# Kernel optimization log

Hardware: AMD Instinct MI355X
Metric: run time of the kernel (lower is better)

Reference implementation:

```python
import jax, jax.numpy as jnp
import numpy as np

B, N, DIM = 4, 1024, 768
H, GP = 12, 64
HD = DIM // H
SCALE = HD ** -0.5


def setup_inputs() -> dict:
    key = jax.random.key(0)
    ks = jax.random.split(key, 7)
    s = DIM ** -0.5
    return {
        "x": jax.random.normal(ks[0], (B, N, DIM), dtype=jnp.float32),
        "W_qkv": jax.random.normal(ks[1], (3 * DIM, DIM), dtype=jnp.float32) * s,
        "b_qkv": jnp.zeros((3 * DIM,), dtype=jnp.float32),
        "W_gp": jax.random.normal(ks[2], (GP, DIM), dtype=jnp.float32) * s,
        "alpha": jax.random.normal(ks[3], (1, H, 1, 1), dtype=jnp.float32),
        "W_proj": jax.random.normal(ks[4], (DIM, DIM), dtype=jnp.float32) * s,
        "b_proj": jnp.zeros((DIM,), dtype=jnp.float32),
    }


def reference(x, W_qkv, b_qkv, W_gp, alpha, W_proj, b_proj):
    b, n, c = x.shape
    # qkv projection, split into heads: [b, h, n, hd]
    qkv = x @ W_qkv.T + b_qkv
    q, k, v = jnp.split(qkv, 3, axis=-1)
    def to_heads(t):
        return t.reshape(b, n, H, HD).transpose(0, 2, 1, 3)
    q, k, v = to_heads(q), to_heads(k), to_heads(v)

    # raw attention scores [b, h, n, n]
    attn = jnp.einsum('bhnd,bhmd->bhnm', q, k) * SCALE

    # group similarity: gp weight viewed as [h, gp, hd]
    gp = W_gp.reshape(H, GP, HD)
    gw = jnp.einsum('bhnd,hmd->bhnm', v, gp)          # [b, h, n, gp]
    gw = jax.nn.gelu(gw, approximate=False)           # exact GELU (torch default)
    gw = jax.nn.softmax(gw, axis=-1)
    G = jnp.einsum('bhnm,bhkm->bhnk', gw, gw)         # [b, h, n, n]

    # gated combination
    attn = jax.nn.softmax(attn * G, axis=-1)
    a = jax.nn.sigmoid(alpha)                          # [1, h, 1, 1]
    A = (1.0 - a) * attn + a * G
    # column-sum renormalization (sum over query dim 2)
    A = A / (A.sum(axis=2, keepdims=True) + 1e-8)

    out = jnp.einsum('bhnm,bhmd->bhnd', A, v)
    out = out.transpose(0, 2, 1, 3).reshape(b, n, c)
    return out @ W_proj.T + b_proj
```

## Files before the change

### kernel.cpp

```cpp
#include <hip/hip_runtime.h>
#include <math.h>

namespace {

constexpr int kN   = 1024;
constexpr int kDim = 768;
constexpr int kH   = 12;
constexpr int kBH  = 48;
constexpr float kScale = 0.125f;

typedef __attribute__((ext_vector_type(8))) short short8;
typedef __attribute__((ext_vector_type(4))) short short4v;
typedef __attribute__((ext_vector_type(4))) float f32x4;
typedef __attribute__((ext_vector_type(16))) float f32x16;
typedef __attribute__((ext_vector_type(4))) uint uint4v;
typedef _Float16 f16x8 __attribute__((ext_vector_type(8)));

#define MFMA(a, b, c)      __builtin_amdgcn_mfma_f32_16x16x32_bf16(a, b, c, 0, 0, 0)
#define MFMA32(a, b, c)    __builtin_amdgcn_mfma_f32_32x32x16_bf16(a, b, c, 0, 0, 0)
#define MFMA32F16(a, b, c) __builtin_amdgcn_mfma_f32_32x32x16_f16(a, b, c, 0, 0, 0)

__device__ __forceinline__ ushort f2bf(float f) {
  uint u = __builtin_bit_cast(uint, f);
  u += 0x7fffu + ((u >> 16) & 1u);
  return (ushort)(u >> 16);
}
__device__ __forceinline__ float bf2f(ushort h) {
  uint u = ((uint)h) << 16;
  return __builtin_bit_cast(float, u);
}
__device__ __forceinline__ void split8(const float* f, short8& hi, short8& lo) {
  #pragma unroll
  for (int i = 0; i < 8; i++) {
    const ushort h = f2bf(f[i]);
    hi[i] = (short)h;
    lo[i] = (short)f2bf(f[i] - bf2f(h));
  }
}
__device__ __forceinline__ uint packbf(float a, float b) {
  return (uint)f2bf(a) | ((uint)f2bf(b) << 16);
}
__device__ __forceinline__ ushort f2h(float f) {
  return __builtin_bit_cast(ushort, (_Float16)f);
}

__device__ __forceinline__ void gl16(const void* g, void* l) {
  __builtin_amdgcn_global_load_lds(
      (const __attribute__((address_space(1))) void*)g,
      (__attribute__((address_space(3))) void*)l, 16, 0, 0);
}

__device__ __forceinline__ short8 frag(const short* t, int row, int chunk) {
  return *(const short8*)(t + row * 64 + ((chunk ^ (row & 7)) << 3));
}

template<int ROWS, int W>
__device__ __forceinline__ void stage_tile(short* dst, const short* src,
                                           int stride, int w, int l) {
  #pragma unroll
  for (int c = 0; c < ROWS / 8; c += W) {
    const int cc = c + w;
    const int row0 = cc << 3;
    const int row = row0 + (l >> 3);
    const int ch = (l & 7) ^ (row & 7);
    gl16(src + (size_t)row * stride + (ch << 3), dst + row0 * 64);
  }
}

__global__ __launch_bounds__(256) void k_split(const float* __restrict__ src,
                                               short* __restrict__ h,
                                               short* __restrict__ l) {
  const size_t i = ((size_t)blockIdx.x * 256 + threadIdx.x) * 4;
  const float4 f = *(const float4*)(src + i);
  const float ff[4] = {f.x, f.y, f.z, f.w};
  short4v hv, lv;
  #pragma unroll
  for (int j = 0; j < 4; j++) {
    const ushort u = f2bf(ff[j]);
    hv[j] = (short)u;
    lv[j] = (short)f2bf(ff[j] - bf2f(u));
  }
  *(short4v*)(h + i) = hv;
  *(short4v*)(l + i) = lv;
}

__global__ __launch_bounds__(512) void k_qkv(const short* __restrict__ xh,
                                             const short* __restrict__ xl,
                                             const short* __restrict__ wh,
                                             const short* __restrict__ wl,
                                             const float* __restrict__ bias,
                                             short* __restrict__ qh, short* __restrict__ ql,
                                             short* __restrict__ kh, short* __restrict__ kl,
                                             short* __restrict__ vh, short* __restrict__ vl) {
  __shared__ __align__(16) short sb[32768];
  const int bx = blockIdx.x, by = blockIdx.y;
  const int tid = threadIdx.x, w = tid >> 6, lane = tid & 63;
  const int wr = w >> 2, wc = w & 3;
  const short* Asrc_h = xh + (size_t)(by * 128) * kDim;
  const short* Asrc_l = xl + (size_t)(by * 128) * kDim;
  const short* Bsrc_h = wh + (size_t)(bx * 128) * kDim;
  const short* Bsrc_l = wl + (size_t)(bx * 128) * kDim;

  f32x4 acc[4][2] = {};
  #pragma unroll 1
  for (int t = 0; t < 12; ++t) {
    const int k0 = t * 64;
    __syncthreads();
    stage_tile<128, 8>(sb,         Asrc_h + k0, kDim, w, lane);
    stage_tile<128, 8>(sb + 8192,  Asrc_l + k0, kDim, w, lane);
    stage_tile<128, 8>(sb + 16384, Bsrc_h + k0, kDim, w, lane);
    stage_tile<128, 8>(sb + 24576, Bsrc_l + k0, kDim, w, lane);
    __syncthreads();
    #pragma unroll
    for (int s = 0; s < 2; ++s) {
      const int ch = (s << 2) + (lane >> 4);
      short8 af[4], alf[4], bf_[2], blf[2];
      #pragma unroll
      for (int i = 0; i < 4; i++) {
        const int ar = wr * 64 + i * 16 + (lane & 15);
        af[i]  = frag(sb, ar, ch);
        alf[i] = frag(sb + 8192, ar, ch);
      }
      #pragma unroll
      for (int j = 0; j < 2; j++) {
        const int br = wc * 32 + j * 16 + (lane & 15);
        bf_[j] = frag(sb + 16384, br, ch);
        blf[j] = frag(sb + 24576, br, ch);
      }
      #pragma unroll
      for (int i = 0; i < 4; i++)
        #pragma unroll
        for (int j = 0; j < 2; j++) {
          acc[i][j] = MFMA(af[i], bf_[j], acc[i][j]);
          acc[i][j] = MFMA(af[i], blf[j], acc[i][j]);
          acc[i][j] = MFMA(alf[i], bf_[j], acc[i][j]);
        }
    }
  }
  #pragma unroll
  for (int j = 0; j < 2; j++) {
    const int col = bx * 128 + wc * 32 + j * 16 + (lane & 15);
    const int part = col / 768;
    const int rem = col - part * 768;
    const int hh = rem >> 6, d = rem & 63;
    short* dh = (part == 0) ? qh : ((part == 1) ? kh : vh);
    short* dl = (part == 0) ? ql : ((part == 1) ? kl : vl);
    const float bv = bias[col];
    const float scl = (part == 0) ? kScale : 1.0f;
    #pragma unroll
    for (int i = 0; i < 4; i++) {
      #pragma unroll
      for (int r = 0; r < 4; r++) {
        const int gr = by * 128 + wr * 64 + i * 16 + ((lane >> 4) << 2) + r;
        const int b = gr >> 10, n = gr & 1023;
        const float val = (acc[i][j][r] + bv) * scl;
        const ushort hu = f2bf(val);
        const size_t idx = (size_t)((b * kH + hh) * kN + n) * 64 + d;
        dh[idx] = (short)hu;
        dl[idx] = (short)f2bf(val - bf2f(hu));
      }
    }
  }
}

__global__ __launch_bounds__(512) void k_gw(const short* __restrict__ vh,
                                            const short* __restrict__ vl,
                                            const float* __restrict__ Wgp,
                                            short* __restrict__ gwh,
                                            short* __restrict__ gwl) {
  const int bh = blockIdx.x;
  const int h = bh % kH;
  const int n0 = blockIdx.y << 7;
  const int tid = threadIdx.x, w = tid >> 6, lane = tid & 63;
  __shared__ __align__(16) short gph[4096], gpl[4096];
  {
    const int r = tid >> 3, c = tid & 7;
    float f[8] __attribute__((aligned(16)));
    *(float4*)(f + 0) = *(const float4*)(Wgp + h * 4096 + r * 64 + c * 8);
    *(float4*)(f + 4) = *(const float4*)(Wgp + h * 4096 + r * 64 + c * 8 + 4);
    short8 hh, ll;
    split8(f, hh, ll);
    const int slot = c ^ (r & 7);
    *(short8*)(gph + r * 64 + slot * 8) = hh;
    *(short8*)(gpl + r * 64 + slot * 8) = ll;
  }
  short8 vhf[2], vlf[2];
  const size_t arow = (size_t)(bh * kN + n0 + w * 16 + (lane & 15)) * 64 + ((lane >> 4) << 3);
  vhf[0] = *(const short8*)(vh + arow); vhf[1] = *(const short8*)(vh + arow + 32);
  vlf[0] = *(const short8*)(vl + arow); vlf[1] = *(const short8*)(vl + arow + 32);
  __syncthreads();

  f32x4 aU[4] = {};
  #pragma unroll
  for (int msub = 0; msub < 4; msub++) {
    #pragma unroll
    for (int s = 0; s < 2; s++) {
      const int row = (msub << 4) + (lane & 15);
      const int ch = (s << 2) + (lane >> 4);
      const short8 bh_ = frag(gph, row, ch);
      const short8 bl_ = frag(gpl, row, ch);
      aU[msub] = MFMA(vhf[s], bh_, aU[msub]);
      aU[msub] = MFMA(vhf[s], bl_, aU[msub]);
      aU[msub] = MFMA(vlf[s], bh_, aU[msub]);
    }
  }
  #pragma unroll
  for (int r = 0; r < 4; r++) {
    float u[4];
    #pragma unroll
    for (int m = 0; m < 4; m++) {
      const float a = aU[m][r];
      u[m] = 0.5f * a * (1.0f + erff(a * 0.70710678118654752f));
    }
    float mx = fmaxf(fmaxf(u[0], u[1]), fmaxf(u[2], u[3]));
    #pragma unroll
    for (int msk = 1; msk < 16; msk <<= 1) mx = fmaxf(mx, __shfl_xor(mx, msk));
    float e[4], ssum = 0.f;
    #pragma unroll
    for (int m = 0; m < 4; m++) { e[m] = __expf(u[m] - mx); ssum += e[m]; }
    #pragma unroll
    for (int msk = 1; msk < 16; msk <<= 1) ssum += __shfl_xor(ssum, msk);
    const float inv = 1.0f / ssum;
    const int n = n0 + w * 16 + ((lane >> 4) << 2) + r;
    #pragma unroll
    for (int m = 0; m < 4; m++) {
      const float g = e[m] * inv;
      const ushort hu = f2bf(g);
      const size_t idx = (size_t)(bh * kN + n) * 64 + (m << 4) + (lane & 15);
      gwh[idx] = (short)hu;
      gwl[idx] = (short)f2bf(g - bf2f(hu));
    }
  }
}

template<int F16>
__global__ __launch_bounds__(256) void k_vt(const short* __restrict__ vh,
                                            const float* __restrict__ rcolv,
                                            short* __restrict__ vtg) {
  const int bh = blockIdx.x;
  const int n0 = blockIdx.y << 6;
  __shared__ short t[64][80];
  const int tid = threadIdx.x;
  {
    const int n = tid >> 2, d0 = (tid & 3) << 4;
    const float rc = rcolv[bh * kN + n0 + n];
    const short8 a = *(const short8*)(vh + (size_t)(bh * kN + n0 + n) * 64 + d0);
    const short8 b = *(const short8*)(vh + (size_t)(bh * kN + n0 + n) * 64 + d0 + 8);
    #pragma unroll
    for (int i = 0; i < 8; ++i) {
      const float v0 = bf2f((ushort)a[i]) * rc;
      const float v1 = bf2f((ushort)b[i]) * rc;
      t[d0 + i][n]     = F16 ? (short)f2h(v0) : (short)f2bf(v0);
      t[d0 + 8 + i][n] = F16 ? (short)f2h(v1) : (short)f2bf(v1);
    }
  }
  __syncthreads();
  const int d = tid >> 2, j0 = (tid & 3) << 4;
  short* dst = vtg + (size_t)bh * 65536 + (size_t)d * 1024 + n0 + j0;
  *(short8*)(dst)     = *(const short8*)(&t[d][j0]);
  *(short8*)(dst + 8) = *(const short8*)(&t[d][j0 + 8]);
}

__global__ __launch_bounds__(256, 3) void k_denom(const short* __restrict__ qh,
                                                  const short* __restrict__ ql,
                                                  const short* __restrict__ kh,
                                                  const short* __restrict__ kl,
                                                  const short* __restrict__ gwh,
                                                  const short* __restrict__ gwl,
                                                  float* __restrict__ rdenom) {
  const int bh = blockIdx.x;
  const int n0 = blockIdx.y << 6;
  const int tid = threadIdx.x, w = tid >> 6, lane = tid & 63;
  const int lc = lane & 31, hl = lane >> 5;
  const int nw = w & 1, mh = w >> 1;
  __shared__ __align__(16) short sb[16384];
  __shared__ float part[4][32];

  short8 qB[4], qlB[4], gB[4], glB[4];
  {
    const size_t nrow = (size_t)(bh * kN + n0 + nw * 32 + lc) * 64;
    #pragma unroll
    for (int ks = 0; ks < 4; ks++) {
      const int off = ks * 16 + (hl << 3);
      qB[ks]  = *(const short8*)(qh  + nrow + off);
      qlB[ks] = *(const short8*)(ql  + nrow + off);
      gB[ks]  = *(const short8*)(gwh + nrow + off);
      glB[ks] = *(const short8*)(gwl + nrow + off);
    }
  }
  float dsum = 0.f;
  #pragma unroll 1
  for (int t = 0; t < 16; ++t) {
    __syncthreads();
    const size_t mo0 = (size_t)(bh * kN + t * 32) * 64;
    const size_t mo1 = (size_t)(bh * kN + 512 + t * 32) * 64;
    stage_tile<32, 4>(sb,                kh  + mo0, 64, w, lane);
    stage_tile<32, 4>(sb + 2048,         kh  + mo1, 64, w, lane);
    stage_tile<32, 4>(sb + 4096,         kl  + mo0, 64, w, lane);
    stage_tile<32, 4>(sb + 4096 + 2048,  kl  + mo1, 64, w, lane);
    stage_tile<32, 4>(sb + 8192,         gwh + mo0, 64, w, lane);
    stage_tile<32, 4>(sb + 8192 + 2048,  gwh + mo1, 64, w, lane);
    stage_tile<32, 4>(sb + 12288,        gwl + mo0, 64, w, lane);
    stage_tile<32, 4>(sb + 12288 + 2048, gwl + mo1, 64, w, lane);
    __syncthreads();
    f32x16 aS = {}, aG = {};
    #pragma unroll
    for (int ks = 0; ks < 4; ++ks) {
      const int row = mh * 32 + lc;
      const int ck = ks * 2 + hl;
      const short8 Ah_ = frag(sb, row, ck);
      const short8 Al_ = frag(sb + 4096, row, ck);
      const short8 Eh_ = frag(sb + 8192, row, ck);
      const short8 El_ = frag(sb + 12288, row, ck);
      aS = MFMA32(Ah_, qB[ks], aS);
      aS = MFMA32(Al_, qB[ks], aS);
      aS = MFMA32(Ah_, qlB[ks], aS);
      aG = MFMA32(Eh_, gB[ks], aG);
      aG = MFMA32(El_, gB[ks], aG);
      aG = MFMA32(Eh_, glB[ks], aG);
    }
    #pragma unroll
    for (int r = 0; r < 16; ++r)
      dsum += __expf(aS[r] * aG[r]);
  }
  dsum += __shfl_xor(dsum, 32);
  if (hl == 0) part[w][lc] = dsum;
  __syncthreads();
  if (tid < 64)
    rdenom[bh * kN + n0 + tid] =
        1.0f / (part[tid >> 5][tid & 31] + part[2 + (tid >> 5)][tid & 31]);
}

template<int WA>
__global__ __launch_bounds__(256, 3) void k_colsum(const short* __restrict__ qh,
                                                   const short* __restrict__ ql,
                                                   const short* __restrict__ kh,
                                                   const short* __restrict__ kl,
                                                   const short* __restrict__ gwh,
                                                   const short* __restrict__ gwl,
                                                   const float* __restrict__ rdenom,
                                                   const float* __restrict__ alpha,
                                                   float* __restrict__ rcolv,
                                                   ushort* __restrict__ Ab) {
  const int bh = blockIdx.x;
  const int m0 = blockIdx.y << 6;
  const int tid = threadIdx.x, w = tid >> 6, lane = tid & 63;
  const int lc = lane & 31, hl = lane >> 5;
  const int mw = w & 1, nh = w >> 1;
  __shared__ __align__(16) short sb[16384];
  __shared__ float part[4][32];
  __shared__ float rdl[2][32];
  const float ah_ = 1.0f / (1.0f + __expf(-alpha[bh % kH]));
  const float om = 1.0f - ah_;
  const int m_g = m0 + mw * 32 + lc;
  ushort* Arow = WA ? (Ab + ((size_t)bh << 20) + m_g) : nullptr;

  short8 kB[4], klB[4], gB[4], glB[4];
  {
    const size_t mrow = (size_t)(bh * kN + m_g) * 64;
    #pragma unroll
    for (int ks = 0; ks < 4; ks++) {
      const int off = ks * 16 + (hl << 3);
      kB[ks]  = *(const short8*)(kh  + mrow + off);
      klB[ks] = *(const short8*)(kl  + mrow + off);
      gB[ks]  = *(const short8*)(gwh + mrow + off);
      glB[ks] = *(const short8*)(gwl + mrow + off);
    }
  }
  float csum = 0.f;
  #pragma unroll 1
  for (int t = 0; t < 16; ++t) {
    __syncthreads();
    const size_t no0 = (size_t)(bh * kN + t * 32) * 64;
    const size_t no1 = (size_t)(bh * kN + 512 + t * 32) * 64;
    stage_tile<32, 4>(sb,                qh  + no0, 64, w, lane);
    stage_tile<32, 4>(sb + 2048,         qh  + no1, 64, w, lane);
    stage_tile<32, 4>(sb + 4096,         ql  + no0, 64, w, lane);
    stage_tile<32, 4>(sb + 4096 + 2048,  ql  + no1, 64, w, lane);
    stage_tile<32, 4>(sb + 8192,         gwh + no0, 64, w, lane);
    stage_tile<32, 4>(sb + 8192 + 2048,  gwh + no1, 64, w, lane);
    stage_tile<32, 4>(sb + 12288,        gwl + no0, 64, w, lane);
    stage_tile<32, 4>(sb + 12288 + 2048, gwl + no1, 64, w, lane);
    if (tid < 64)
      rdl[tid >> 5][tid & 31] =
          rdenom[bh * kN + (tid >> 5) * 512 + t * 32 + (tid & 31)];
    __syncthreads();
    f32x16 aS = {}, aG = {};
    #pragma unroll
    for (int ks = 0; ks < 4; ++ks) {
      const int row = nh * 32 + lc;
      const int ck = ks * 2 + hl;
      const short8 Ah_ = frag(sb, row, ck);
      const short8 Al_ = frag(sb + 4096, row, ck);
      const short8 Eh_ = frag(sb + 8192, row, ck);
      const short8 El_ = frag(sb + 12288, row, ck);
      aS = MFMA32(Ah_, kB[ks], aS);
      aS = MFMA32(Al_, kB[ks], aS);
      aS = MFMA32(Ah_, klB[ks], aS);
      aG = MFMA32(Eh_, gB[ks], aG);
      aG = MFMA32(El_, gB[ks], aG);
      aG = MFMA32(Eh_, glB[ks], aG);
    }
    #pragma unroll
    for (int r = 0; r < 16; ++r) {
      const int nr = (r & 3) + ((r >> 2) << 3) + (hl << 2);
      const float g = aG[r];
      const float a = om * (__expf(aS[r] * g) * rdl[nh][nr]) + ah_ * g;
      csum += a;
      if (WA) {
        const int n_g = nh * 512 + t * 32 + nr;
        Arow[(size_t)n_g << 10] = f2h(a);
      }
    }
  }
  csum += __shfl_xor(csum, 32);
  if (hl == 0) part[w][lc] = csum;
  __syncthreads();
  if (tid < 64)
    rcolv[bh * kN + m0 + tid] =
        1.0f / (part[tid >> 5][tid & 31] + part[2 + (tid >> 5)][tid & 31] + 1e-8f);
}

__global__ __launch_bounds__(256) void k_outA(const ushort* __restrict__ Ab,
                                              const short* __restrict__ vtf,
                                              short* __restrict__ ctxh,
                                              short* __restrict__ ctxl) {
  const int bh = blockIdx.x;
  const int h = bh % kH;
  const int b = bh / kH;
  const int n0 = blockIdx.y << 6;
  const int tid = threadIdx.x, w = tid >> 6, lane = tid & 63;
  const int lc = lane & 31, hl = lane >> 5;
  const int nw = w & 1, mh = w >> 1;
  __shared__ __align__(16) short sbm[10240];
  short* At = sbm;
  short* Vt = sbm + 4096;
  const ushort* Abh = Ab + ((size_t)bh << 20);
  const short* Vbh = vtf + ((size_t)bh << 16);
  f32x16 oac[2] = {};

  #pragma unroll 1
  for (int t = 0; t < 16; ++t) {
    __syncthreads();
    #pragma unroll
    for (int c = 0; c < 8; c += 4) {
      const int cc = c + w;
      const int row0 = cc << 3;
      const int row = row0 + (lane >> 3);
      const int ce = (lane & 7) ^ (row & 7);
      const int mg = ((ce >> 2) ? 512 : 0) + t * 32 + ((ce & 3) << 3);
      gl16(Abh + ((size_t)(n0 + row) << 10) + mg, At + row0 * 64);
      gl16(Vbh + ((size_t)row << 10) + mg, Vt + row0 * 64);
    }
    __syncthreads();
    #pragma unroll
    for (int dt = 0; dt < 2; ++dt)
      #pragma unroll
      for (int ks = 0; ks < 2; ++ks) {
        const int ck = mh * 4 + ks * 2 + hl;
        const f16x8 va = __builtin_bit_cast(f16x8, frag(Vt, dt * 32 + lc, ck));
        const f16x8 pe = __builtin_bit_cast(f16x8, frag(At, nw * 32 + lc, ck));
        oac[dt] = MFMA32F16(va, pe, oac[dt]);
      }
  }
  __syncthreads();
  float* buf = (float*)sbm;
  if (mh == 1) {
    #pragma unroll
    for (int dt = 0; dt < 2; ++dt)
      #pragma unroll
      for (int r = 0; r < 16; ++r) {
        const int d = dt * 32 + (r & 3) + ((r >> 2) << 3) + (hl << 2);
        buf[(nw * 32 + lc) * 68 + d] = oac[dt][r];
      }
  }
  __syncthreads();
  if (mh == 0) {
    #pragma unroll
    for (int dt = 0; dt < 2; ++dt)
      #pragma unroll
      for (int r = 0; r < 16; ++r) {
        const int d = dt * 32 + (r & 3) + ((r >> 2) << 3) + (hl << 2);
        const int idx = (nw * 32 + lc) * 68 + d;
        buf[idx] = oac[dt][r] + buf[idx];
      }
  }
  __syncthreads();
  {
    const int rowi = tid >> 2;
    const int d0 = (tid & 3) << 4;
    float f[16] __attribute__((aligned(16)));
    #pragma unroll
    for (int j = 0; j < 4; ++j)
      *(float4*)(f + 4 * j) = *(const float4*)(&buf[rowi * 68 + d0 + 4 * j]);
    const int n = n0 + rowi;
    short* dsth = ctxh + (size_t)(b * kN + n) * kDim + h * 64 + d0;
    short* dstl = ctxl + (size_t)(b * kN + n) * kDim + h * 64 + d0;
    #pragma unroll
    for (int g8 = 0; g8 < 2; ++g8) {
      short8 hi, lo;
      split8(f + 8 * g8, hi, lo);
      *(short8*)(dsth + 8 * g8) = hi;
      *(short8*)(dstl + 8 * g8) = lo;
    }
  }
}

__global__ __launch_bounds__(256, 3) void k_out9(const short* __restrict__ qh,
                                                 const short* __restrict__ ql,
                                                 const short* __restrict__ kh,
                                                 const short* __restrict__ kl,
                                                 const short* __restrict__ vtg,
                                                 const short* __restrict__ gwh,
                                                 const short* __restrict__ gwl,
                                                 const float* __restrict__ rdenom,
                                                 const float* __restrict__ alpha,
                                                 short* __restrict__ ctxh,
                                                 short* __restrict__ ctxl) {
  const int bh = blockIdx.x;
  const int h = bh % kH;
  const int b = bh / kH;
  const int n0 = blockIdx.y << 6;
  const int tid = threadIdx.x, w = tid >> 6, lane = tid & 63;
  const int lc = lane & 31, hl = lane >> 5;
  const int nw = w & 1, mh = w >> 1;
  __shared__ __align__(16) short sb[20480];
  const float ah_ = 1.0f / (1.0f + __expf(-alpha[h]));
  const float om = 1.0f - ah_;

  short8 qB[4], qlB[4], gB[4], glB[4];
  {
    const size_t nrow = (size_t)(bh * kN + n0 + nw * 32 + lc) * 64;
    #pragma unroll
    for (int ks = 0; ks < 4; ks++) {
      const int off = ks * 16 + (hl << 3);
      qB[ks]  = *(const short8*)(qh  + nrow + off);
      qlB[ks] = *(const short8*)(ql  + nrow + off);
      gB[ks]  = *(const short8*)(gwh + nrow + off);
      glB[ks] = *(const short8*)(gwl + nrow + off);
    }
  }
  const float rdn = rdenom[bh * kN + n0 + nw * 32 + lc];
  const short* vbh = vtg + (size_t)bh * 65536;
  f32x16 oac[2] = {};

  #pragma unroll 1
  for (int t = 0; t < 16; ++t) {
    __syncthreads();
    const size_t mo0 = (size_t)(bh * kN + t * 32) * 64;
    const size_t mo1 = (size_t)(bh * kN + 512 + t * 32) * 64;
    stage_tile<32, 4>(sb,                kh  + mo0, 64, w, lane);
    stage_tile<32, 4>(sb + 2048,         kh  + mo1, 64, w, lane);
    stage_tile<32, 4>(sb + 4096,         kl  + mo0, 64, w, lane);
    stage_tile<32, 4>(sb + 4096 + 2048,  kl  + mo1, 64, w, lane);
    stage_tile<32, 4>(sb + 8192,         gwh + mo0, 64, w, lane);
    stage_tile<32, 4>(sb + 8192 + 2048,  gwh + mo1, 64, w, lane);
    stage_tile<32, 4>(sb + 12288,        gwl + mo0, 64, w, lane);
    stage_tile<32, 4>(sb + 12288 + 2048, gwl + mo1, 64, w, lane);
    #pragma unroll
    for (int c = 0; c < 8; c += 4) {
      const int cc = c + w;
      const int row0 = cc << 3;
      const int row = row0 + (lane >> 3);
      const int ch = (lane & 7) ^ (row & 7);
      const int mg = ((ch >> 2) ? 512 : 0) + t * 32 + ((ch & 3) << 3);
      gl16(vbh + (size_t)row * 1024 + mg, sb + 16384 + row0 * 64);
    }
    __syncthreads();
    f32x16 aS = {}, aG = {};
    #pragma unroll
    for (int ks = 0; ks < 4; ++ks) {
      const int row = mh * 32 + lc;
      const int ck = ks * 2 + hl;
      const short8 Ah_ = frag(sb, row, ck);
      const short8 Al_ = frag(sb + 4096, row, ck);
      const short8 Eh_ = frag(sb + 8192, row, ck);
      const short8 El_ = frag(sb + 12288, row, ck);
      aS = MFMA32(Ah_, qB[ks], aS);
      aS = MFMA32(Al_, qB[ks], aS);
      aS = MFMA32(Ah_, qlB[ks], aS);
      aG = MFMA32(Eh_, gB[ks], aG);
      aG = MFMA32(El_, gB[ks], aG);
      aG = MFMA32(Eh_, glB[ks], aG);
    }
    float a[16];
    #pragma unroll
    for (int r = 0; r < 16; ++r) {
      const float g = aG[r];
      const float p = __expf(aS[r] * g) * rdn;
      a[r] = om * p + ah_ * g;
    }
    short8 pf[2];
    {
      uint W[8], Ws[8];
      #pragma unroll
      for (int j = 0; j < 8; ++j) W[j] = packbf(a[2 * j], a[2 * j + 1]);
      #pragma unroll
      for (int j = 0; j < 8; ++j) Ws[j] = __shfl_xor(W[j], 32);
      uint4v b0, b1;
      b0[0] = hl ? Ws[2] : W[0];  b0[1] = hl ? Ws[3] : W[1];
      b0[2] = hl ? W[2]  : Ws[0]; b0[3] = hl ? W[3]  : Ws[1];
      b1[0] = hl ? Ws[6] : W[4];  b1[1] = hl ? Ws[7] : W[5];
      b1[2] = hl ? W[6]  : Ws[4]; b1[3] = hl ? W[7]  : Ws[5];
      pf[0] = __builtin_bit_cast(short8, b0);
      pf[1] = __builtin_bit_cast(short8, b1);
    }
    #pragma unroll
    for (int dt = 0; dt < 2; ++dt)
      #pragma unroll
      for (int ks = 0; ks < 2; ++ks) {
        const short8 va = frag(sb + 16384, dt * 32 + lc, mh * 4 + ks * 2 + hl);
        oac[dt] = MFMA32(va, pf[ks], oac[dt]);
      }
  }
  __syncthreads();
  float* buf = (float*)sb;
  if (mh == 1) {
    #pragma unroll
    for (int dt = 0; dt < 2; ++dt)
      #pragma unroll
      for (int r = 0; r < 16; ++r) {
        const int d = dt * 32 + (r & 3) + ((r >> 2) << 3) + (hl << 2);
        buf[(nw * 32 + lc) * 68 + d] = oac[dt][r];
      }
  }
  __syncthreads();
  if (mh == 0) {
    #pragma unroll
    for (int dt = 0; dt < 2; ++dt)
      #pragma unroll
      for (int r = 0; r < 16; ++r) {
        const int d = dt * 32 + (r & 3) + ((r >> 2) << 3) + (hl << 2);
        const int idx = (nw * 32 + lc) * 68 + d;
        buf[idx] = oac[dt][r] + buf[idx];
      }
  }
  __syncthreads();
  {
    const int rowi = tid >> 2;
    const int d0 = (tid & 3) << 4;
    float f[16] __attribute__((aligned(16)));
    #pragma unroll
    for (int j = 0; j < 4; ++j)
      *(float4*)(f + 4 * j) = *(const float4*)(&buf[rowi * 68 + d0 + 4 * j]);
    const int n = n0 + rowi;
    short* dsth = ctxh + (size_t)(b * kN + n) * kDim + h * 64 + d0;
    short* dstl = ctxl + (size_t)(b * kN + n) * kDim + h * 64 + d0;
    #pragma unroll
    for (int g8 = 0; g8 < 2; ++g8) {
      short8 hi, lo;
      split8(f + 8 * g8, hi, lo);
      *(short8*)(dsth + 8 * g8) = hi;
      *(short8*)(dstl + 8 * g8) = lo;
    }
  }
}

__global__ __launch_bounds__(512) void k_proj(const short* __restrict__ ch_,
                                              const short* __restrict__ cl_,
                                              const short* __restrict__ wh,
                                              const short* __restrict__ wl,
                                              const float* __restrict__ bias,
                                              float* __restrict__ out) {
  __shared__ __align__(16) short sb[2][32768];
  const int bx = blockIdx.x, by = blockIdx.y;
  const int tid = threadIdx.x, w = tid >> 6, lane = tid & 63;
  const int wr = w >> 2, wc = w & 3;
  const short* Asrc_h = ch_ + (size_t)(by * 128) * kDim;
  const short* Asrc_l = cl_ + (size_t)(by * 128) * kDim;
  const short* Bsrc_h = wh + (size_t)(bx * 128) * kDim;
  const short* Bsrc_l = wl + (size_t)(bx * 128) * kDim;

  f32x4 acc[4][2] = {};
  {
    short* nb = sb[0];
    stage_tile<128, 8>(nb,         Asrc_h, kDim, w, lane);
    stage_tile<128, 8>(nb + 8192,  Asrc_l, kDim, w, lane);
    stage_tile<128, 8>(nb + 16384, Bsrc_h, kDim, w, lane);
    stage_tile<128, 8>(nb + 24576, Bsrc_l, kDim, w, lane);
  }
  int p = 0;
  #pragma unroll 1
  for (int t = 0; t < 12; ++t) {
    __syncthreads();
    if (t < 11) {
      const int k0 = (t + 1) * 64;
      short* nb = sb[p ^ 1];
      stage_tile<128, 8>(nb,         Asrc_h + k0, kDim, w, lane);
      stage_tile<128, 8>(nb + 8192,  Asrc_l + k0, kDim, w, lane);
      stage_tile<128, 8>(nb + 16384, Bsrc_h + k0, kDim, w, lane);
      stage_tile<128, 8>(nb + 24576, Bsrc_l + k0, kDim, w, lane);
    }
    const short* cb = sb[p];
    #pragma unroll
    for (int s = 0; s < 2; ++s) {
      const int ch = (s << 2) + (lane >> 4);
      short8 af[4], alf[4], bf_[2], blf[2];
      #pragma unroll
      for (int i = 0; i < 4; i++) {
        const int ar = wr * 64 + i * 16 + (lane & 15);
        af[i]  = frag(cb, ar, ch);
        alf[i] = frag(cb + 8192, ar, ch);
      }
      #pragma unroll
      for (int j = 0; j < 2; j++) {
        const int br = wc * 32 + j * 16 + (lane & 15);
        bf_[j] = frag(cb + 16384, br, ch);
        blf[j] = frag(cb + 24576, br, ch);
      }
      #pragma unroll
      for (int i = 0; i < 4; i++)
        #pragma unroll
        for (int j = 0; j < 2; j++) {
          acc[i][j] = MFMA(af[i], bf_[j], acc[i][j]);
          acc[i][j] = MFMA(af[i], blf[j], acc[i][j]);
          acc[i][j] = MFMA(alf[i], bf_[j], acc[i][j]);
          acc[i][j] = MFMA(alf[i], blf[j], acc[i][j]);
        }
    }
    p ^= 1;
  }
  #pragma unroll
  for (int j = 0; j < 2; j++) {
    const int col = bx * 128 + wc * 32 + j * 16 + (lane & 15);
    const float bv = bias[col];
    #pragma unroll
    for (int i = 0; i < 4; i++) {
      #pragma unroll
      for (int r = 0; r < 4; r++) {
        const int row = by * 128 + wr * 64 + i * 16 + ((lane >> 4) << 2) + r;
        out[(size_t)row * kDim + col] = acc[i][j][r] + bv;
      }
    }
  }
}

}

extern "C" void kernel_launch(void* const* d_in, const int* in_sizes, int n_in,
                              void* d_out, int out_size, void* d_ws, size_t ws_size,
                              hipStream_t stream) {
  const float* x     = (const float*)d_in[0];
  const float* Wqkv  = (const float*)d_in[1];
  const float* bqkv  = (const float*)d_in[2];
  const float* Wgp   = (const float*)d_in[3];
  const float* alpha = (const float*)d_in[4];
  const float* Wproj = (const float*)d_in[5];
  const float* bproj = (const float*)d_in[6];
  float* out = (float*)d_out;

  const size_t he = 3145728;
  short* qh  = (short*)d_ws;
  short* ql  = qh + he;
  short* kh  = ql + he;
  short* kl  = kh + he;
  short* vh  = kl + he;
  short* vl  = vh + he;
  short* gwh = vl + he;
  short* gwl = gwh + he;
  short* xh  = gwl + he;
  short* xl  = xh + he;
  float* rdenom = (float*)(xl + he);
  float* rcolv  = rdenom + (size_t)kBH * kN;
  ushort* Ab    = (ushort*)(rcolv + (size_t)kBH * kN);
  const size_t need_mat = (size_t)(rcolv + (size_t)kBH * kN - (float*)d_ws) * 4
                        + (size_t)kBH * kN * kN * 2;
  const bool mat = ws_size >= need_mat;

  short* Wqh = gwh;  short* Wql = gwl;
  short* vt  = vl;
  short* ctxh = xh;  short* ctxl = xl;
  short* Wph = qh;   short* Wpl = ql;

  k_split<<<3072, 256, 0, stream>>>(x, xh, xl);
  k_split<<<1728, 256, 0, stream>>>(Wqkv, Wqh, Wql);
  k_qkv  <<<dim3(18, 32), 512, 0, stream>>>(xh, xl, Wqh, Wql, bqkv,
                                            qh, ql, kh, kl, vh, vl);
  k_gw   <<<dim3(kBH, 8), 512, 0, stream>>>(vh, vl, Wgp, gwh, gwl);
  k_denom<<<dim3(kBH, 16), 256, 0, stream>>>(qh, ql, kh, kl, gwh, gwl, rdenom);
  if (mat) {
    k_colsum<1><<<dim3(kBH, 16), 256, 0, stream>>>(qh, ql, kh, kl, gwh, gwl,
                                                   rdenom, alpha, rcolv, Ab);
    k_vt<1> <<<dim3(kBH, 16), 256, 0, stream>>>(vh, rcolv, vt);
    k_outA  <<<dim3(kBH, 16), 256, 0, stream>>>(Ab, vt, ctxh, ctxl);
  } else {
    k_colsum<0><<<dim3(kBH, 16), 256, 0, stream>>>(qh, ql, kh, kl, gwh, gwl,
                                                   rdenom, alpha, rcolv, nullptr);
    k_vt<0> <<<dim3(kBH, 16), 256, 0, stream>>>(vh, rcolv, vt);
    k_out9  <<<dim3(kBH, 16), 256, 0, stream>>>(qh, ql, kh, kl, vt, gwh, gwl,
                                                rdenom, alpha, ctxh, ctxl);
  }
  k_split<<<576, 256, 0, stream>>>(Wproj, Wph, Wpl);
  k_proj <<<dim3(6, 32), 512, 0, stream>>>(ctxh, ctxl, Wph, Wpl, bproj, out);
}
```

Baseline: 228.9 us.

## Store exp scores once and factor the G term through a low-rank product

The materialized path now has the denominator pass write unnormalized exp(S*G) scores in fp16 and per-block column partials. This replaces the second full QK/G recomputation that the column-sum kernel used to do. The column normalizer is built from those partials plus a closed-form sum over G using the gw column sums. In the output, the alpha*G*V term is factored as gw·(gw^T·V') via a small per-head 64x64 matrix M, so it no longer goes through the n×n matrix. The cost is extra kernels (transpose, rcol, M), an fp16 exp matrix that uses a fixed -4 shift and could overflow or underflow, and a re-read of E for the column partials.

```diff
diff --git a/kernel.cpp b/kernel.cpp
--- a/kernel.cpp
+++ b/kernel.cpp
@@ -42,6 +42,9 @@
 }
 __device__ __forceinline__ ushort f2h(float f) {
   return __builtin_bit_cast(ushort, (_Float16)f);
+}
+__device__ __forceinline__ float h2f(ushort u) {
+  return (float)__builtin_bit_cast(_Float16, u);
 }
 
 __device__ __forceinline__ void gl16(const void* g, void* l) {
@@ -167,7 +170,8 @@
                                             const short* __restrict__ vl,
                                             const float* __restrict__ Wgp,
                                             short* __restrict__ gwh,
-                                            short* __restrict__ gwl) {
+                                            short* __restrict__ gwl,
+                                            short* __restrict__ gwf) {
   const int bh = blockIdx.x;
   const int h = bh % kH;
   const int n0 = blockIdx.y << 7;
@@ -229,8 +233,36 @@
       const size_t idx = (size_t)(bh * kN + n) * 64 + (m << 4) + (lane & 15);
       gwh[idx] = (short)hu;
       gwl[idx] = (short)f2bf(g - bf2f(hu));
-    }
-  }
+      if (gwf) gwf[idx] = (short)f2h(g);
+    }
+  }
+}
+
+__global__ __launch_bounds__(256) void k_gwt(const short* __restrict__ gwh,
+                                             const short* __restrict__ gwl,
+                                             short* __restrict__ gwt) {
+  const int bh = blockIdx.x;
+  const int n0 = blockIdx.y << 6;
+  __shared__ short t[64][80];
+  const int tid = threadIdx.x;
+  {
+    const int n = tid >> 2, k0 = (tid & 3) << 4;
+    const size_t row = (size_t)(bh * kN + n0 + n) * 64 + k0;
+    const short8 h0 = *(const short8*)(gwh + row);
+    const short8 h1 = *(const short8*)(gwh + row + 8);
+    const short8 l0 = *(const short8*)(gwl + row);
+    const short8 l1 = *(const short8*)(gwl + row + 8);
+    #pragma unroll
+    for (int i = 0; i < 8; ++i) {
+      t[k0 + i][n]     = (short)f2h(bf2f((ushort)h0[i]) + bf2f((ushort)l0[i]));
+      t[k0 + 8 + i][n] = (short)f2h(bf2f((ushort)h1[i]) + bf2f((ushort)l1[i]));
+    }
+  }
+  __syncthreads();
+  const int k = tid >> 2, j0 = (tid & 3) << 4;
+  short* dst = gwt + ((size_t)bh << 16) + (size_t)k * 1024 + n0 + j0;
+  *(short8*)(dst)     = *(const short8*)(&t[k][j0]);
+  *(short8*)(dst + 8) = *(const short8*)(&t[k][j0 + 8]);
 }
 
 template<int F16>
@@ -259,6 +291,312 @@
   short* dst = vtg + (size_t)bh * 65536 + (size_t)d * 1024 + n0 + j0;
   *(short8*)(dst)     = *(const short8*)(&t[d][j0]);
   *(short8*)(dst + 8) = *(const short8*)(&t[d][j0 + 8]);
+}
+
+__global__ __launch_bounds__(256, 3) void k_denomE(const short* __restrict__ qh,
+                                                   const short* __restrict__ ql,
+                                                   const short* __restrict__ kh,
+                                                   const short* __restrict__ kl,
+                                                   const short* __restrict__ gwh,
+                                                   const short* __restrict__ gwl,
+                                                   float* __restrict__ rdenom,
+                                                   ushort* __restrict__ Eb,
+                                                   float* __restrict__ partials) {
+  const int bh = blockIdx.x;
+  const int blk = blockIdx.y;
+  const int n0 = blk << 6;
+  const int tid = threadIdx.x, w = tid >> 6, lane = tid & 63;
+  const int lc = lane & 31, hl = lane >> 5;
+  const int nw = w & 1, mh = w >> 1;
+  __shared__ __align__(16) short sb[16384];
+  __shared__ float part[4][32];
+  __shared__ float rdl[64];
+
+  short8 qB[4], qlB[4], gB[4], glB[4];
+  {
+    const size_t nrow = (size_t)(bh * kN + n0 + nw * 32 + lc) * 64;
+    #pragma unroll
+    for (int ks = 0; ks < 4; ks++) {
+      const int off = ks * 16 + (hl << 3);
+      qB[ks]  = *(const short8*)(qh  + nrow + off);
+      qlB[ks] = *(const short8*)(ql  + nrow + off);
+      gB[ks]  = *(const short8*)(gwh + nrow + off);
+      glB[ks] = *(const short8*)(gwl + nrow + off);
+    }
+  }
+  ushort* Ebh = Eb + ((size_t)bh << 20);
+  float dsum[16] = {};
+  #pragma unroll 1
+  for (int t = 0; t < 16; ++t) {
+    __syncthreads();
+    const size_t mo0 = (size_t)(bh * kN + t * 32) * 64;
+    const size_t mo1 = (size_t)(bh * kN + 512 + t * 32) * 64;
+    stage_tile<32, 4>(sb,                kh  + mo0, 64, w, lane);
+    stage_tile<32, 4>(sb + 2048,         kh  + mo1, 64, w, lane);
+    stage_tile<32, 4>(sb + 4096,         kl  + mo0, 64, w, lane);
+    stage_tile<32, 4>(sb + 4096 + 2048,  kl  + mo1, 64, w, lane);
+    stage_tile<32, 4>(sb + 8192,         gwh + mo0, 64, w, lane);
+    stage_tile<32, 4>(sb + 8192 + 2048,  gwh + mo1, 64, w, lane);
+    stage_tile<32, 4>(sb + 12288,        gwl + mo0, 64, w, lane);
+    stage_tile<32, 4>(sb + 12288 + 2048, gwl + mo1, 64, w, lane);
+    __syncthreads();
+    f32x16 aS = {}, aG = {};
+    #pragma unroll
+    for (int ks = 0; ks < 4; ++ks) {
+      const int row = mh * 32 + lc;
+      const int ck = ks * 2 + hl;
+      const short8 Ah_ = frag(sb, row, ck);
+      const short8 Al_ = frag(sb + 4096, row, ck);
+      const short8 Eh_ = frag(sb + 8192, row, ck);
+      const short8 El_ = frag(sb + 12288, row, ck);
+      aS = MFMA32(qB[ks], Ah_, aS);
+      aS = MFMA32(qB[ks], Al_, aS);
+      aS = MFMA32(qlB[ks], Ah_, aS);
+      aG = MFMA32(gB[ks], Eh_, aG);
+      aG = MFMA32(gB[ks], El_, aG);
+      aG = MFMA32(glB[ks], Eh_, aG);
+    }
+    const int m = mh * 512 + t * 32 + lc;
+    #pragma unroll
+    for (int r = 0; r < 16; ++r) {
+      const int nl = (r & 3) + ((r >> 2) << 3) + (hl << 2);
+      const float e = __expf(aS[r] * aG[r] - 4.0f);
+      dsum[r] += e;
+      Ebh[((size_t)(n0 + nw * 32 + nl) << 10) + m] = f2h(e);
+    }
+  }
+  #pragma unroll
+  for (int r = 0; r < 16; ++r)
+    #pragma unroll
+    for (int msk = 1; msk < 32; msk <<= 1)
+      dsum[r] += __shfl_xor(dsum[r], msk);
+  if (lc == 0) {
+    #pragma unroll
+    for (int r = 0; r < 16; ++r)
+      part[w][(r & 3) + ((r >> 2) << 3) + (hl << 2)] = dsum[r];
+  }
+  __syncthreads();
+  if (tid < 64) {
+    const float v = 1.0f / (part[tid >> 5][tid & 31] + part[(tid >> 5) + 2][tid & 31]);
+    rdenom[bh * kN + n0 + tid] = v;
+    rdl[tid] = v;
+  }
+  __syncthreads();
+  {
+    const int m4 = tid << 2;
+    float a0 = 0.f, a1 = 0.f, a2 = 0.f, a3 = 0.f;
+    #pragma unroll 4
+    for (int n = 0; n < 64; ++n) {
+      const short4v ev = *(const short4v*)((const short*)Ebh + ((size_t)(n0 + n) << 10) + m4);
+      const float rv = rdl[n];
+      a0 = fmaf(h2f((ushort)ev[0]), rv, a0);
+      a1 = fmaf(h2f((ushort)ev[1]), rv, a1);
+      a2 = fmaf(h2f((ushort)ev[2]), rv, a2);
+      a3 = fmaf(h2f((ushort)ev[3]), rv, a3);
+    }
+    *(float4*)(partials + (((size_t)(bh * 16 + blk)) << 10) + m4) =
+        make_float4(a0, a1, a2, a3);
+  }
+}
+
+__global__ __launch_bounds__(256) void k_rcol(const short* __restrict__ gwh,
+                                              const short* __restrict__ gwl,
+                                              const float* __restrict__ partials,
+                                              const float* __restrict__ alpha,
+                                              float* __restrict__ rcolv) {
+  const int bh = blockIdx.x;
+  const int tid = threadIdx.x;
+  const float ah_ = 1.0f / (1.0f + __expf(-alpha[bh % kH]));
+  const float om = 1.0f - ah_;
+  __shared__ float sgp[4][64];
+  __shared__ float sgw[64];
+  {
+    const int k = tid & 63, grp = tid >> 6;
+    float s = 0.f;
+    const size_t base = (size_t)bh * kN * 64 + k;
+    for (int n = grp * 256; n < grp * 256 + 256; ++n) {
+      s += bf2f((ushort)gwh[base + (size_t)n * 64]) +
+           bf2f((ushort)gwl[base + (size_t)n * 64]);
+    }
+    sgp[grp][k] = s;
+  }
+  __syncthreads();
+  if (tid < 64) sgw[tid] = sgp[0][tid] + sgp[1][tid] + sgp[2][tid] + sgp[3][tid];
+  __syncthreads();
+  #pragma unroll
+  for (int j = 0; j < 4; ++j) {
+    const int m = tid * 4 + j;
+    float cp = 0.f;
+    #pragma unroll
+    for (int b2 = 0; b2 < 16; ++b2)
+      cp += partials[(((size_t)(bh * 16 + b2)) << 10) + m];
+    float gd = 0.f;
+    const short* gh = gwh + (size_t)(bh * kN + m) * 64;
+    const short* gl2 = gwl + (size_t)(bh * kN + m) * 64;
+    #pragma unroll 16
+    for (int k = 0; k < 64; ++k)
+      gd += sgw[k] * (bf2f((ushort)gh[k]) + bf2f((ushort)gl2[k]));
+    rcolv[bh * kN + m] = 1.0f / (om * cp + ah_ * gd + 1e-8f);
+  }
+}
+
+__global__ __launch_bounds__(256) void k_M(const short* __restrict__ vtf,
+                                           const short* __restrict__ gwt,
+                                           ushort* __restrict__ Mt) {
+  const int bh = blockIdx.x;
+  const int tid = threadIdx.x, w = tid >> 6, lane = tid & 63;
+  const int lc = lane & 31, hl = lane >> 5;
+  __shared__ float red[4][32][32];
+  const short* Vb = vtf + ((size_t)bh << 16);
+  const short* Gb = gwt + ((size_t)bh << 16);
+  f32x16 acc00 = {}, acc01 = {}, acc10 = {}, acc11 = {};
+  #pragma unroll 1
+  for (int mc = 0; mc < 16; ++mc) {
+    const int m0 = w * 256 + mc * 16 + hl * 8;
+    const f16x8 v0 = __builtin_bit_cast(f16x8, *(const short8*)(Vb + (size_t)(lc) * 1024 + m0));
+    const f16x8 v1 = __builtin_bit_cast(f16x8, *(const short8*)(Vb + (size_t)(32 + lc) * 1024 + m0));
+    const f16x8 g0 = __builtin_bit_cast(f16x8, *(const short8*)(Gb + (size_t)(lc) * 1024 + m0));
+    const f16x8 g1 = __builtin_bit_cast(f16x8, *(const short8*)(Gb + (size_t)(32 + lc) * 1024 + m0));
+    acc00 = MFMA32F16(v0, g0, acc00);
+    acc01 = MFMA32F16(v0, g1, acc01);
+    acc10 = MFMA32F16(v1, g0, acc10);
+    acc11 = MFMA32F16(v1, g1, acc11);
+  }
+  #pragma unroll 1
+  for (int q = 0; q < 4; ++q) {
+    const int dt = q >> 1, kt = q & 1;
+    const f32x16 a = (q == 0) ? acc00 : ((q == 1) ? acc01 : ((q == 2) ? acc10 : acc11));
+    __syncthreads();
+    #pragma unroll
+    for (int r = 0; r < 16; ++r)
+      red[w][(r & 3) + ((r >> 2) << 3) + (hl << 2)][lc] = a[r];
+    __syncthreads();
+    for (int i = tid; i < 1024; i += 256) {
+      const int dr = i >> 5, kc = i & 31;
+      const float v = red[0][dr][kc] + red[1][dr][kc] + red[2][dr][kc] + red[3][dr][kc];
+      Mt[(size_t)bh * 4096 + (size_t)(dt * 32 + dr) * 64 + kt * 32 + kc] = f2h(v);
+    }
+  }
+}
+
+__global__ __launch_bounds__(256) void k_outA2(const ushort* __restrict__ Eb,
+                                               const short* __restrict__ vtf,
+                                               const short* __restrict__ gwf,
+                                               const ushort* __restrict__ Mt,
+                                               const float* __restrict__ rdenom,
+                                               const float* __restrict__ alpha,
+                                               short* __restrict__ ctxh,
+                                               short* __restrict__ ctxl) {
+  const int bh = blockIdx.x;
+  const int h = bh % kH;
+  const int b = bh / kH;
+  const int n0 = blockIdx.y << 6;
+  const int tid = threadIdx.x, w = tid >> 6, lane = tid & 63;
+  const int lc = lane & 31, hl = lane >> 5;
+  const int nw = w & 1, mh = w >> 1;
+  __shared__ __align__(16) short sbm[10240];
+  short* At = sbm;
+  short* Vt = sbm + 4096;
+  const ushort* Ebh = Eb + ((size_t)bh << 20);
+  const short* Vbh = vtf + ((size_t)bh << 16);
+  const float ah_ = 1.0f / (1.0f + __expf(-alpha[h]));
+  const float om = 1.0f - ah_;
+  const float rdn = rdenom[bh * kN + n0 + nw * 32 + lc];
+  f32x16 oac[2] = {};
+
+  #pragma unroll 1
+  for (int t = 0; t < 16; ++t) {
+    __syncthreads();
+    #pragma unroll
+    for (int c = 0; c < 8; c += 4) {
+      const int cc = c + w;
+      const int row0 = cc << 3;
+      const int row = row0 + (lane >> 3);
+      const int ce = (lane & 7) ^ (row & 7);
+      const int mg = ((ce >> 2) ? 512 : 0) + t * 32 + ((ce & 3) << 3);
+      gl16(Ebh + ((size_t)(n0 + row) << 10) + mg, At + row0 * 64);
+      gl16(Vbh + ((size_t)row << 10) + mg, Vt + row0 * 64);
+    }
+    __syncthreads();
+    #pragma unroll
+    for (int dt = 0; dt < 2; ++dt)
+      #pragma unroll
+      for (int ks = 0; ks < 2; ++ks) {
+        const int ck = mh * 4 + ks * 2 + hl;
+        const f16x8 va = __builtin_bit_cast(f16x8, frag(Vt, dt * 32 + lc, ck));
+        const f16x8 pe = __builtin_bit_cast(f16x8, frag(At, nw * 32 + lc, ck));
+        oac[dt] = MFMA32F16(va, pe, oac[dt]);
+      }
+  }
+  const float s1 = om * rdn;
+  #pragma unroll
+  for (int dt = 0; dt < 2; ++dt)
+    #pragma unroll
+    for (int r = 0; r < 16; ++r)
+      oac[dt][r] *= s1;
+  __syncthreads();
+  stage_tile<64, 4>(At, (const short*)Mt + (size_t)bh * 4096, 64, w, lane);
+  short8 gB2[2];
+  {
+    const short* gr = gwf + (size_t)(bh * kN + n0 + nw * 32 + lc) * 64;
+    gB2[0] = *(const short8*)(gr + (mh * 2 + 0) * 16 + hl * 8);
+    gB2[1] = *(const short8*)(gr + (mh * 2 + 1) * 16 + hl * 8);
+  }
+  __syncthreads();
+  f32x16 o2[2] = {};
+  #pragma unroll
+  for (int dt = 0; dt < 2; ++dt)
+    #pragma unroll
+    for (int s = 0; s < 2; ++s) {
+      const f16x8 ma = __builtin_bit_cast(f16x8, frag(At, dt * 32 + lc, (mh * 2 + s) * 2 + hl));
+      o2[dt] = MFMA32F16(ma, __builtin_bit_cast(f16x8, gB2[s]), o2[dt]);
+    }
+  #pragma unroll
+  for (int dt = 0; dt < 2; ++dt)
+    #pragma unroll
+    for (int r = 0; r < 16; ++r)
+      oac[dt][r] = fmaf(ah_, o2[dt][r], oac[dt][r]);
+  __syncthreads();
+  float* buf = (float*)sbm;
+  if (mh == 1) {
+    #pragma unroll
+    for (int dt = 0; dt < 2; ++dt)
+      #pragma unroll
+      for (int r = 0; r < 16; ++r) {
+        const int d = dt * 32 + (r & 3) + ((r >> 2) << 3) + (hl << 2);
+        buf[(nw * 32 + lc) * 68 + d] = oac[dt][r];
+      }
+  }
+  __syncthreads();
+  if (mh == 0) {
+    #pragma unroll
+    for (int dt = 0; dt < 2; ++dt)
+      #pragma unroll
+      for (int r = 0; r < 16; ++r) {
+        const int d = dt * 32 + (r & 3) + ((r >> 2) << 3) + (hl << 2);
+        const int idx = (nw * 32 + lc) * 68 + d;
+        buf[idx] = oac[dt][r] + buf[idx];
+      }
+  }
+  __syncthreads();
+  {
+    const int rowi = tid >> 2;
+    const int d0 = (tid & 3) << 4;
+    float f[16] __attribute__((aligned(16)));
+    #pragma unroll
+    for (int j = 0; j < 4; ++j)
+      *(float4*)(f + 4 * j) = *(const float4*)(&buf[rowi * 68 + d0 + 4 * j]);
+    const int n = n0 + rowi;
+    short* dsth = ctxh + (size_t)(b * kN + n) * kDim + h * 64 + d0;
+    short* dstl = ctxl + (size_t)(b * kN + n) * kDim + h * 64 + d0;
+    #pragma unroll
+    for (int g8 = 0; g8 < 2; ++g8) {
+      short8 hi, lo;
+      split8(f + 8 * g8, hi, lo);
+      *(short8*)(dsth + 8 * g8) = hi;
+      *(short8*)(dstl + 8 * g8) = lo;
+    }
+  }
 }
 
 __global__ __launch_bounds__(256, 3) void k_denom(const short* __restrict__ qh,
@@ -331,7 +669,6 @@
         1.0f / (part[tid >> 5][tid & 31] + part[2 + (tid >> 5)][tid & 31]);
 }
 
-template<int WA>
 __global__ __launch_bounds__(256, 3) void k_colsum(const short* __restrict__ qh,
                                                    const short* __restrict__ ql,
                                                    const short* __restrict__ kh,
@@ -340,8 +677,7 @@
                                                    const short* __restrict__ gwl,
                                                    const float* __restrict__ rdenom,
                                                    const float* __restrict__ alpha,
-                                                   float* __restrict__ rcolv,
-                                                   ushort* __restrict__ Ab) {
+                                                   float* __restrict__ rcolv) {
   const int bh = blockIdx.x;
   const int m0 = blockIdx.y << 6;
   const int tid = threadIdx.x, w = tid >> 6, lane = tid & 63;
@@ -352,12 +688,10 @@
   __shared__ float rdl[2][32];
   const float ah_ = 1.0f / (1.0f + __expf(-alpha[bh % kH]));
   const float om = 1.0f - ah_;
-  const int m_g = m0 + mw * 32 + lc;
-  ushort* Arow = WA ? (Ab + ((size_t)bh << 20) + m_g) : nullptr;
 
   short8 kB[4], klB[4], gB[4], glB[4];
   {
-    const size_t mrow = (size_t)(bh * kN + m_g) * 64;
+    const size_t mrow = (size_t)(bh * kN + m0 + mw * 32 + lc) * 64;
     #pragma unroll
     for (int ks = 0; ks < 4; ks++) {
       const int off = ks * 16 + (hl << 3);
@@ -405,12 +739,7 @@
     for (int r = 0; r < 16; ++r) {
       const int nr = (r & 3) + ((r >> 2) << 3) + (hl << 2);
       const float g = aG[r];
-      const float a = om * (__expf(aS[r] * g) * rdl[nh][nr]) + ah_ * g;
-      csum += a;
-      if (WA) {
-        const int n_g = nh * 512 + t * 32 + nr;
-        Arow[(size_t)n_g << 10] = f2h(a);
-      }
+      csum += om * (__expf(aS[r] * g) * rdl[nh][nr]) + ah_ * g;
     }
   }
   csum += __shfl_xor(csum, 32);
@@ -419,91 +748,6 @@
   if (tid < 64)
     rcolv[bh * kN + m0 + tid] =
         1.0f / (part[tid >> 5][tid & 31] + part[2 + (tid >> 5)][tid & 31] + 1e-8f);
-}
-
-__global__ __launch_bounds__(256) void k_outA(const ushort* __restrict__ Ab,
-                                              const short* __restrict__ vtf,
-                                              short* __restrict__ ctxh,
-                                              short* __restrict__ ctxl) {
-  const int bh = blockIdx.x;
-  const int h = bh % kH;
-  const int b = bh / kH;
-  const int n0 = blockIdx.y << 6;
-  const int tid = threadIdx.x, w = tid >> 6, lane = tid & 63;
-  const int lc = lane & 31, hl = lane >> 5;
-  const int nw = w & 1, mh = w >> 1;
-  __shared__ __align__(16) short sbm[10240];
-  short* At = sbm;
-  short* Vt = sbm + 4096;
-  const ushort* Abh = Ab + ((size_t)bh << 20);
-  const short* Vbh = vtf + ((size_t)bh << 16);
-  f32x16 oac[2] = {};
-
-  #pragma unroll 1
-  for (int t = 0; t < 16; ++t) {
-    __syncthreads();
-    #pragma unroll
-    for (int c = 0; c < 8; c += 4) {
-      const int cc = c + w;
-      const int row0 = cc << 3;
-      const int row = row0 + (lane >> 3);
-      const int ce = (lane & 7) ^ (row & 7);
-      const int mg = ((ce >> 2) ? 512 : 0) + t * 32 + ((ce & 3) << 3);
-      gl16(Abh + ((size_t)(n0 + row) << 10) + mg, At + row0 * 64);
-      gl16(Vbh + ((size_t)row << 10) + mg, Vt + row0 * 64);
-    }
-    __syncthreads();
-    #pragma unroll
-    for (int dt = 0; dt < 2; ++dt)
-      #pragma unroll
-      for (int ks = 0; ks < 2; ++ks) {
-        const int ck = mh * 4 + ks * 2 + hl;
-        const f16x8 va = __builtin_bit_cast(f16x8, frag(Vt, dt * 32 + lc, ck));
-        const f16x8 pe = __builtin_bit_cast(f16x8, frag(At, nw * 32 + lc, ck));
-        oac[dt] = MFMA32F16(va, pe, oac[dt]);
-      }
-  }
-  __syncthreads();
-  float* buf = (float*)sbm;
-  if (mh == 1) {
-    #pragma unroll
-    for (int dt = 0; dt < 2; ++dt)
-      #pragma unroll
-      for (int r = 0; r < 16; ++r) {
-        const int d = dt * 32 + (r & 3) + ((r >> 2) << 3) + (hl << 2);
-        buf[(nw * 32 + lc) * 68 + d] = oac[dt][r];
-      }
-  }
-  __syncthreads();
-  if (mh == 0) {
-    #pragma unroll
-    for (int dt = 0; dt < 2; ++dt)
-      #pragma unroll
-      for (int r = 0; r < 16; ++r) {
-        const int d = dt * 32 + (r & 3) + ((r >> 2) << 3) + (hl << 2);
-        const int idx = (nw * 32 + lc) * 68 + d;
-        buf[idx] = oac[dt][r] + buf[idx];
-      }
-  }
-  __syncthreads();
-  {
-    const int rowi = tid >> 2;
-    const int d0 = (tid & 3) << 4;
-    float f[16] __attribute__((aligned(16)));
-    #pragma unroll
-    for (int j = 0; j < 4; ++j)
-      *(float4*)(f + 4 * j) = *(const float4*)(&buf[rowi * 68 + d0 + 4 * j]);
-    const int n = n0 + rowi;
-    short* dsth = ctxh + (size_t)(b * kN + n) * kDim + h * 64 + d0;
-    short* dstl = ctxl + (size_t)(b * kN + n) * kDim + h * 64 + d0;
-    #pragma unroll
-    for (int g8 = 0; g8 < 2; ++g8) {
-      short8 hi, lo;
-      split8(f + 8 * g8, hi, lo);
-      *(short8*)(dsth + 8 * g8) = hi;
-      *(short8*)(dstl + 8 * g8) = lo;
-    }
-  }
 }
 
 __global__ __launch_bounds__(256, 3) void k_out9(const short* __restrict__ qh,
@@ -762,10 +1006,13 @@
   short* xl  = xh + he;
   float* rdenom = (float*)(xl + he);
   float* rcolv  = rdenom + (size_t)kBH * kN;
-  ushort* Ab    = (ushort*)(rcolv + (size_t)kBH * kN);
-  const size_t need_mat = (size_t)(rcolv + (size_t)kBH * kN - (float*)d_ws) * 4
-                        + (size_t)kBH * kN * kN * 2;
-  const bool mat = ws_size >= need_mat;
+  ushort* Eb    = (ushort*)(rcolv + (size_t)kBH * kN);
+  float* partials = (float*)(Eb + (size_t)kBH * kN * kN);
+  ushort* Mt    = (ushort*)(partials + (size_t)kBH * 16 * kN);
+  short* gwt    = (short*)(Mt + (size_t)kBH * 64 * 64);
+  short* gwf    = gwt + (size_t)kBH * 64 * kN;
+  const size_t need = (size_t)((char*)(gwf + (size_t)kBH * kN * 64) - (char*)d_ws);
+  const bool mat = ws_size >= need;
 
   short* Wqh = gwh;  short* Wql = gwl;
   short* vt  = vl;
@@ -776,16 +1023,21 @@
   k_split<<<1728, 256, 0, stream>>>(Wqkv, Wqh, Wql);
   k_qkv  <<<dim3(18, 32), 512, 0, stream>>>(xh, xl, Wqh, Wql, bqkv,
                                             qh, ql, kh, kl, vh, vl);
-  k_gw   <<<dim3(kBH, 8), 512, 0, stream>>>(vh, vl, Wgp, gwh, gwl);
-  k_denom<<<dim3(kBH, 16), 256, 0, stream>>>(qh, ql, kh, kl, gwh, gwl, rdenom);
+  k_gw   <<<dim3(kBH, 8), 512, 0, stream>>>(vh, vl, Wgp, gwh, gwl,
+                                            mat ? gwf : nullptr);
   if (mat) {
-    k_colsum<1><<<dim3(kBH, 16), 256, 0, stream>>>(qh, ql, kh, kl, gwh, gwl,
-                                                   rdenom, alpha, rcolv, Ab);
+    k_gwt   <<<dim3(kBH, 16), 256, 0, stream>>>(gwh, gwl, gwt);
+    k_denomE<<<dim3(kBH, 16), 256, 0, stream>>>(qh, ql, kh, kl, gwh, gwl,
+                                                rdenom, Eb, partials);
+    k_rcol  <<<kBH, 256, 0, stream>>>(gwh, gwl, partials, alpha, rcolv);
     k_vt<1> <<<dim3(kBH, 16), 256, 0, stream>>>(vh, rcolv, vt);
-    k_outA  <<<dim3(kBH, 16), 256, 0, stream>>>(Ab, vt, ctxh, ctxl);
+    k_M     <<<kBH, 256, 0, stream>>>(vt, gwt, Mt);
+    k_outA2 <<<dim3(kBH, 16), 256, 0, stream>>>(Eb, vt, gwf, Mt, rdenom,
+                                                alpha, ctxh, ctxl);
   } else {
-    k_colsum<0><<<dim3(kBH, 16), 256, 0, stream>>>(qh, ql, kh, kl, gwh, gwl,
-                                                   rdenom, alpha, rcolv, nullptr);
+    k_denom <<<dim3(kBH, 16), 256, 0, stream>>>(qh, ql, kh, kl, gwh, gwl, rdenom);
+    k_colsum<<<dim3(kBH, 16), 256, 0, stream>>>(qh, ql, kh, kl, gwh, gwl,
+                                                rdenom, alpha, rcolv);
     k_vt<0> <<<dim3(kBH, 16), 256, 0, stream>>>(vh, rcolv, vt);
     k_out9  <<<dim3(kBH, 16), 256, 0, stream>>>(qh, ql, kh, kl, vt, gwh, gwl,
                                                 rdenom, alpha, ctxh, ctxl);
```

After: 240.4 us, median of 2. +5.0%, slower.
